# Optimization experiments

Hardware: AMD Instinct MI355X
Metric: run time of the kernel (lower is better)

Reference implementation:

```python
import math
import jax, jax.numpy as jnp
import numpy as np

COULOMB = 14.399645478425668  # eV*Angstrom / e^2


def setup_inputs() -> dict:
    key = jax.random.key(0)
    k0, k1, k2, k3, k4 = jax.random.split(key, 5)
    B, n, F, S = 128, 512, 64, 4  # molecules, atoms/molecule, feat dim, n species
    N = B * n
    node_features = jax.random.normal(k0, (N, F), dtype=jnp.float32)
    pos = jax.random.normal(k1, (N, 3), dtype=jnp.float32) * 5.0  # spread atoms out
    atom_type = jax.random.randint(k2, (N,), 0, S)
    total_charge = jnp.zeros((B, 1), dtype=jnp.float32)
    chi_weight = jax.random.normal(k3, (F, 1), dtype=jnp.float32) / np.float32(np.sqrt(F))
    hardness_param = jnp.ones((S,), dtype=jnp.float32)
    sigma = 0.3 + 0.5 * jax.random.uniform(k4, (S,), dtype=jnp.float32)  # covalent radii
    return dict(node_features=node_features, pos=pos, atom_type=atom_type,
                total_charge=total_charge, chi_weight=chi_weight,
                hardness_param=hardness_param, sigma=sigma, n_per_mol=n)


def reference(node_features, pos, atom_type, total_charge, chi_weight,
              hardness_param, sigma, n_per_mol):
    n = n_per_mol
    N, F = node_features.shape
    B = N // n

    feats = node_features.reshape(B, n, F)
    pos_b = pos.reshape(B, n, 3)
    sp = atom_type.reshape(B, n)

    chi = (feats @ chi_weight)[..., 0]                      # [B, n] electronegativity
    hard = jnp.square(hardness_param)[sp]                   # [B, n]
    sig = sigma[sp]                                         # [B, n]

    # pairwise distances within each molecule (diag masked for safe divide)
    diff = pos_b[:, :, None, :] - pos_b[:, None, :, :]      # [B, n, n, 3]
    d2 = jnp.sum(diff * diff, axis=-1)
    eye = jnp.eye(n, dtype=pos.dtype)
    d = jnp.sqrt(jnp.where(eye, 1.0, d2))                   # [B, n, n]

    gamma = jnp.sqrt(sig[:, :, None] ** 2 + sig[:, None, :] ** 2)
    off = COULOMB * jax.lax.erf(d / (math.sqrt(2.0) * gamma)) / d
    diag = hard + COULOMB / (math.sqrt(math.pi) * sig)      # [B, n]
    coeffs = off * (1.0 - eye) + eye * diag[:, :, None]     # [B, n, n]

    # augmented Qeq system with charge-conservation Lagrange multiplier
    A = jnp.ones((B, n + 1, n + 1), dtype=coeffs.dtype)
    A = A.at[:, :n, :n].set(coeffs)
    A = A.at[:, n, n].set(0.0)
    rhs = jnp.concatenate([-chi, total_charge], axis=1)     # [B, n+1]
    sol = jnp.linalg.solve(A, rhs[..., None])[..., 0]
    q = sol[:, :n]                                          # [B, n] charges

    # E = sum_{i<j} C_ij q_i q_j + sum_i (chi_i q_i + 0.5 diag_i q_i^2)
    #   = 0.5 q^T C q + chi . q   (C includes diagonal)
    e_qeq = 0.5 * jnp.einsum('bi,bij,bj->b', q, coeffs, q) + jnp.sum(chi * q, axis=1)
    return e_qeq[:, None], q.reshape(N, 1)
```

## Files before the change

### kernel.cpp

```cpp
#include <hip/hip_runtime.h>
#include <math.h>

#define NA 512
#define NN (NA*NA)
#define COULOMB 14.399645478425668f
#define SQRT_PI 1.7724538509055160273f

__device__ __forceinline__ float rl(float x, int lane) {
    return __int_as_float(__builtin_amdgcn_readlane(__float_as_int(x), lane));
}

__device__ __forceinline__ float pair_val(float dx, float dy, float dz,
                                          float s2i, float s2k) {
    float d2 = dx*dx + dy*dy + dz*dz;
    float rinv = rsqrtf(d2);
    return COULOMB * erff(d2 * rinv * rsqrtf(2.f * (s2i + s2k))) * rinv;
}

__global__ void k_pre(const float* __restrict__ feats, const float* __restrict__ w,
                      const int* __restrict__ type, const float* __restrict__ hard,
                      const float* __restrict__ sigma,
                      float* __restrict__ chi, float* __restrict__ diag,
                      float* __restrict__ sigA, int N) {
    __shared__ float wl[64];
    int tid = threadIdx.x;
    if (tid < 64) wl[tid] = w[tid];
    __syncthreads();
    int i = blockIdx.x * 256 + tid;
    if (i >= N) return;
    const float4* fp = (const float4*)(feats + (size_t)i * 64);
    float acc = 0.f;
#pragma unroll
    for (int q = 0; q < 16; q++) {
        float4 v = fp[q];
        acc += v.x * wl[4*q] + v.y * wl[4*q+1] + v.z * wl[4*q+2] + v.w * wl[4*q+3];
    }
    chi[i] = acc;
    int t = type[i];
    float s = sigma[t];
    float h = hard[t];
    sigA[i] = s;
    diag[i] = h * h + COULOMB / (SQRT_PI * s);
}

__global__ void __launch_bounds__(256, 1) k_panel(const float* __restrict__ pos,
                                                  const float* __restrict__ sigA,
                                                  const float* __restrict__ diagA,
                                                  float* __restrict__ C, const int j) {
    const int q = blockIdx.x;
    const int b = blockIdx.y;
    float* __restrict__ Cb = C + (size_t)b * NN;
    const int jb = j * 64;
    const int m = NA - jb - 64;
    const int tid = threadIdx.x;
    __shared__ float D[64 * 65];
    __shared__ float DT[64 * 64];
    __shared__ float invd[64];
    __shared__ float px[NA], py[NA], pz[NA], s2s[NA];

    if (j == 0) {
#pragma unroll
        for (int e = 0; e < 2; e++) {
            int i = e * 256 + tid;
            px[i] = pos[((size_t)b * NA + i) * 3 + 0];
            py[i] = pos[((size_t)b * NA + i) * 3 + 1];
            pz[i] = pos[((size_t)b * NA + i) * 3 + 2];
            float s = sigA[b * NA + i];
            s2s[i] = s * s;
        }
        __syncthreads();
    }

#pragma unroll
    for (int e = 0; e < 16; e++) {
        int f = e * 256 + tid;
        int rr = f >> 6, cc = f & 63;
        float v;
        if (j == 0) {
            if (rr == cc) v = diagA[b * NA + rr];
            else v = pair_val(px[rr]-px[cc], py[rr]-py[cc], pz[rr]-pz[cc], s2s[rr], s2s[cc]);
        } else {
            v = Cb[(size_t)(jb + rr) * NA + jb + cc];
        }
        D[rr * 65 + cc] = v;
    }

    const int h = m >> 1;
    const int r0 = q ? h : 0;
    const int nr = q ? (m - h) : h;
    const int r = tid - 32;
    const bool hasrow = (r >= 0 && r < nr);
    const int grow = jb + 64 + r0 + r;
    float rv[64];
    if (hasrow) {
        if (j == 0) {
#pragma unroll
            for (int k = 0; k < 64; k++)
                rv[k] = pair_val(px[grow]-px[k], py[grow]-py[k], pz[grow]-pz[k],
                                 s2s[grow], s2s[k]);
        } else {
            const float4* rp = (const float4*)(Cb + (size_t)grow * NA + jb);
#pragma unroll
            for (int qq = 0; qq < 16; qq++) {
                float4 v = rp[qq];
                rv[4*qq] = v.x; rv[4*qq+1] = v.y; rv[4*qq+2] = v.z; rv[4*qq+3] = v.w;
            }
        }
    }
    __syncthreads();

    if (tid < 64) {
        const int t = tid;
        float cl[64];
#pragma unroll
        for (int i = 0; i < 64; i++) cl[i] = (i >= t) ? D[i * 65 + t] : D[t * 65 + i];
#pragma unroll
        for (int k = 0; k < 64; k++) {
            float pivot = rl(cl[k], k);
            float invp = 1.0f / pivot;
            float factor = (t > k) ? (cl[k] * invp) : 0.0f;
#pragma unroll
            for (int i = k + 1; i < 64; i++) {
                float bc = rl(cl[i], k);
                cl[i] -= bc * factor;
            }
        }
        float rs = 1.0f / sqrtf(cl[t]);
        invd[t] = rs;
#pragma unroll
        for (int i = 0; i < 64; i++)
            if (i >= t) D[i * 65 + t] = cl[i] * rs;
    }
    __syncthreads();

#pragma unroll
    for (int e = 0; e < 16; e++) {
        int f = e * 256 + tid;
        int row = f >> 6, cc = f & 63;
        float v = D[row * 65 + cc];
        DT[row * 64 + cc] = (cc < row) ? v : 0.f;
        if (q == 0 && cc <= row) Cb[(size_t)(jb + row) * NA + jb + cc] = v;
    }
    __syncthreads();

    if (hasrow) {
#pragma unroll
        for (int k = 0; k < 64; k++) {
            float acc = rv[k];
            const float4* Lr = (const float4*)(DT + k * 64);
            const int k4 = k >> 2;
#pragma unroll
            for (int t4 = 0; t4 < k4; t4++) {
                float4 Lv = Lr[t4];
                acc -= Lv.x * rv[4*t4] + Lv.y * rv[4*t4+1] + Lv.z * rv[4*t4+2] + Lv.w * rv[4*t4+3];
            }
#pragma unroll
            for (int tt = k4 * 4; tt < k; tt++) acc -= DT[k * 64 + tt] * rv[tt];
            rv[k] = acc * invd[k];
        }
        float4* rp = (float4*)(Cb + (size_t)grow * NA + jb);
#pragma unroll
        for (int qq = 0; qq < 16; qq++)
            rp[qq] = make_float4(rv[4*qq], rv[4*qq+1], rv[4*qq+2], rv[4*qq+3]);
    }
}

template<bool GEN>
__global__ void __launch_bounds__(256, 3) k_trail(float* __restrict__ C,
                                                  const float* __restrict__ pos,
                                                  const float* __restrict__ sigA,
                                                  const float* __restrict__ diagA,
                                                  const int j) {
    const int b = blockIdx.y;
    float* __restrict__ Cb = C + (size_t)b * NN;
    const int jb = j * 64;
    const int m = NA - jb - 64;
    int t = blockIdx.x;
    int RI = 0;
    while (t >= RI + 1) { t -= RI + 1; RI++; }
    const int RJ = t;
    const int RB = RI * 128, CB = RJ * 128;
    const int vr = min(128, m - RB);
    const int vc = min(128, m - CB);
    const int tid = threadIdx.x;
    const int rg = tid >> 4, cg = tid & 15;

    __shared__ float As[128 * 65];
    __shared__ float Bs[128 * 65];

    float acc[8][8];

    if (GEN) {
        __shared__ float pAx[128], pAy[128], pAz[128], sA[128], dA[128];
        __shared__ float pBx[128], pBy[128], pBz[128], sB[128];
        if (tid < 128) {
            if (RB + tid < m) {
                int ga = b * NA + jb + 64 + RB + tid;
                pAx[tid] = pos[(size_t)ga * 3 + 0];
                pAy[tid] = pos[(size_t)ga * 3 + 1];
                pAz[tid] = pos[(size_t)ga * 3 + 2];
                float s = sigA[ga]; sA[tid] = s * s;
                dA[tid] = diagA[ga];
            }
        } else {
            int u = tid - 128;
            if (CB + u < m) {
                int gb = b * NA + jb + 64 + CB + u;
                pBx[u] = pos[(size_t)gb * 3 + 0];
                pBy[u] = pos[(size_t)gb * 3 + 1];
                pBz[u] = pos[(size_t)gb * 3 + 2];
                float s = sigA[gb]; sB[u] = s * s;
            }
        }
        __syncthreads();
#pragma unroll
        for (int rr = 0; rr < 8; rr++) {
            int row = rg * 8 + rr;
#pragma unroll
            for (int cc = 0; cc < 8; cc++) {
                int col = cg + 16 * cc;
                if (RB + row == CB + col)
                    acc[rr][cc] = dA[row];
                else
                    acc[rr][cc] = pair_val(pAx[row]-pBx[col], pAy[row]-pBy[col],
                                           pAz[row]-pBz[col], sA[row], sB[col]);
            }
        }
        __syncthreads();
    } else {
        const int GRB = jb + 64 + RB, GCB = jb + 64 + CB;
#pragma unroll
        for (int rr = 0; rr < 8; rr++) {
            int row = rg * 8 + rr;
#pragma unroll
            for (int cc = 0; cc < 8; cc++) {
                int col = cg + 16 * cc;
                acc[rr][cc] = (row < vr && col < vc)
                    ? Cb[(size_t)(GRB + row) * NA + GCB + col] : 0.f;
            }
        }
    }

    const float* Pan = Cb + (size_t)(jb + 64) * NA + jb;
#pragma unroll
    for (int e = 0; e < 8; e++) {
        int f = e * 256 + tid;
        int row = f >> 4, s = f & 15;
        float4 v = make_float4(0.f, 0.f, 0.f, 0.f);
        if (row < vr) v = *(const float4*)(Pan + (size_t)(RB + row) * NA + s * 4);
        As[row * 65 + s * 4 + 0] = v.x;
        As[row * 65 + s * 4 + 1] = v.y;
        As[row * 65 + s * 4 + 2] = v.z;
        As[row * 65 + s * 4 + 3] = v.w;
        float4 u = make_float4(0.f, 0.f, 0.f, 0.f);
        if (row < vc) u = *(const float4*)(Pan + (size_t)(CB + row) * NA + s * 4);
        Bs[row * 65 + s * 4 + 0] = u.x;
        Bs[row * 65 + s * 4 + 1] = u.y;
        Bs[row * 65 + s * 4 + 2] = u.z;
        Bs[row * 65 + s * 4 + 3] = u.w;
    }
    __syncthreads();

#pragma unroll 4
    for (int k = 0; k < 64; k++) {
        float ai[8], bj[8];
#pragma unroll
        for (int rr = 0; rr < 8; rr++) ai[rr] = As[(rg * 8 + rr) * 65 + k];
#pragma unroll
        for (int cc = 0; cc < 8; cc++) bj[cc] = Bs[(cg + 16 * cc) * 65 + k];
#pragma unroll
        for (int rr = 0; rr < 8; rr++)
#pragma unroll
            for (int cc = 0; cc < 8; cc++)
                acc[rr][cc] = fmaf(-ai[rr], bj[cc], acc[rr][cc]);
    }

    const int GRB = jb + 64 + RB, GCB = jb + 64 + CB;
#pragma unroll
    for (int rr = 0; rr < 8; rr++) {
        int row = rg * 8 + rr;
        if (row < vr) {
#pragma unroll
            for (int cc = 0; cc < 8; cc++) {
                int col = cg + 16 * cc;
                if (col < vc)
                    Cb[(size_t)(GRB + row) * NA + GCB + col] = acc[rr][cc];
            }
        }
    }
}

__global__ void __launch_bounds__(512, 1) k_solve2(const float* __restrict__ C,
                                                   const float* __restrict__ chiA,
                                                   float* __restrict__ x1out,
                                                   float* __restrict__ x2out) {
    const int b = blockIdx.x;
    const int rhs = blockIdx.y;
    const float* Cb = C + (size_t)b * NN;
    const int tid = threadIdx.x;
    __shared__ float D[64 * 65];
    __shared__ float r[NA];
    __shared__ float pb[4][NA];

    r[tid] = rhs ? 1.0f : chiA[b * NA + tid];

    const int sub = tid & 7;
    const int rowg = tid >> 3;

    for (int j = 0; j < 8; j++) {
        const int jb = j * 64;
        __syncthreads();
#pragma unroll
        for (int e = 0; e < 8; e++) {
            int f = e * 512 + tid;
            int row = f >> 6, cc = f & 63;
            D[row * 65 + cc] = Cb[(size_t)(jb + row) * NA + jb + cc];
        }
        __syncthreads();
        if (tid < 64) {
            float val = r[jb + tid];
            float idg = 1.0f / D[tid * 65 + tid];
#pragma unroll
            for (int k = 0; k < 64; k++) {
                float yk = rl(val, k) * rl(idg, k);
                if (tid == k) r[jb + k] = yk;
                float lv = (tid > k) ? D[tid * 65 + k] : 0.f;
                val -= lv * yk;
            }
        }
        __syncthreads();
#pragma unroll
        for (int p = 0; p < 7; p++) {
            int g = jb + 64 + p * 64 + rowg;
            if (g < NA) {
                const float4* Lr = (const float4*)(Cb + (size_t)g * NA + jb + sub * 8);
                float4 a0 = Lr[0], a1 = Lr[1];
                int y0 = jb + sub * 8;
                float d1 = a0.x*r[y0]   + a0.y*r[y0+1] + a0.z*r[y0+2] + a0.w*r[y0+3]
                         + a1.x*r[y0+4] + a1.y*r[y0+5] + a1.z*r[y0+6] + a1.w*r[y0+7];
                d1 += __shfl_xor(d1, 1);
                d1 += __shfl_xor(d1, 2);
                d1 += __shfl_xor(d1, 4);
                if (sub == 0) r[g] -= d1;
            }
        }
    }

    const int ii = tid & 127;
    const int gg = tid >> 7;
    for (int j = 7; j >= 0; j--) {
        const int jb = j * 64;
        __syncthreads();
#pragma unroll
        for (int e = 0; e < 8; e++) {
            int f = e * 512 + tid;
            int row = f >> 6, cc = f & 63;
            D[row * 65 + cc] = Cb[(size_t)(jb + row) * NA + jb + cc];
        }
        __syncthreads();
        if (tid < 64) {
            float val = r[jb + tid];
            float idg = 1.0f / D[tid * 65 + tid];
#pragma unroll
            for (int k = 63; k >= 0; k--) {
                float xk = rl(val, k) * rl(idg, k);
                if (tid == k) r[jb + k] = xk;
                float lv = (tid < k) ? D[k * 65 + tid] : 0.f;
                val -= lv * xk;
            }
        }
        __syncthreads();
        if (jb > 0) {
            const int nf4 = jb >> 2;
            float4 s1 = make_float4(0.f, 0.f, 0.f, 0.f);
            if (ii < nf4) {
#pragma unroll
                for (int gq = 0; gq < 16; gq++) {
                    int g = jb + gg * 16 + gq;
                    float x1 = r[g];
                    float4 Lv = *(const float4*)(Cb + (size_t)g * NA + ii * 4);
                    s1.x += Lv.x * x1; s1.y += Lv.y * x1; s1.z += Lv.z * x1; s1.w += Lv.w * x1;
                }
            }
            *(float4*)(&pb[gg][ii * 4]) = s1;
            __syncthreads();
            if (tid < jb)
                r[tid] -= pb[0][tid] + pb[1][tid] + pb[2][tid] + pb[3][tid];
        }
    }
    __syncthreads();

    float* xo = rhs ? x2out : x1out;
    xo[(size_t)b * NA + tid] = r[tid];
}

__global__ void __launch_bounds__(512, 1) k_final(const float* __restrict__ x1,
                                                  const float* __restrict__ x2,
                                                  const float* __restrict__ chiA,
                                                  const float* __restrict__ Qtot,
                                                  float* __restrict__ out, int B) {
    const int b = blockIdx.x;
    const int tid = threadIdx.x;
    __shared__ float red[16];
    __shared__ float muS;

    float v1 = x1[(size_t)b * NA + tid];
    float v2 = x2[(size_t)b * NA + tid];

    float s1p = v1, s2p = v2;
#pragma unroll
    for (int off = 1; off < 64; off <<= 1) {
        s1p += __shfl_xor(s1p, off);
        s2p += __shfl_xor(s2p, off);
    }
    if ((tid & 63) == 0) { red[tid >> 6] = s1p; red[8 + (tid >> 6)] = s2p; }
    __syncthreads();
    if (tid == 0) {
        float s1 = 0.f, s2 = 0.f;
#pragma unroll
        for (int wv = 0; wv < 8; wv++) { s1 += red[wv]; s2 += red[8 + wv]; }
        muS = -(Qtot[b] + s1) / s2;
    }
    __syncthreads();
    float mu = muS;
    float qv = -v1 - mu * v2;
    out[B + (size_t)b * NA + tid] = qv;

    float eacc = chiA[b * NA + tid] * qv;
#pragma unroll
    for (int off = 1; off < 64; off <<= 1) eacc += __shfl_xor(eacc, off);
    __syncthreads();
    if ((tid & 63) == 0) red[tid >> 6] = eacc;
    __syncthreads();
    if (tid == 0) {
        float e = 0.f;
#pragma unroll
        for (int wv = 0; wv < 8; wv++) e += red[wv];
        out[b] = 0.5f * e - 0.5f * mu * Qtot[b];
    }
}

extern "C" void kernel_launch(void* const* d_in, const int* in_sizes, int n_in,
                              void* d_out, int out_size, void* d_ws, size_t ws_size,
                              hipStream_t stream) {
    const int B = in_sizes[3];
    const int N = in_sizes[2];
    const float* feats = (const float*)d_in[0];
    const float* pos   = (const float*)d_in[1];
    const int*   type  = (const int*)d_in[2];
    const float* Qt    = (const float*)d_in[3];
    const float* w     = (const float*)d_in[4];
    const float* hard  = (const float*)d_in[5];
    const float* sig   = (const float*)d_in[6];
    float* out = (float*)d_out;
    float* ws  = (float*)d_ws;

    float* C    = ws;
    float* chi  = ws + (size_t)B * NN;
    float* diag = chi + N;
    float* sigA = diag + N;

    k_pre<<<(N + 255) / 256, 256, 0, stream>>>(feats, w, type, hard, sig, chi, diag, sigA, N);

    static const int tilesJ[7] = {10, 6, 6, 3, 3, 1, 1};
    for (int j = 0; j < 8; j++) {
        k_panel<<<dim3(2, B), 256, 0, stream>>>(pos, sigA, diag, C, j);
        if (j < 7) {
            if (j == 0)
                k_trail<true><<<dim3(tilesJ[j], B), 256, 0, stream>>>(C, pos, sigA, diag, j);
            else
                k_trail<false><<<dim3(tilesJ[j], B), 256, 0, stream>>>(C, pos, sigA, diag, j);
        }
    }
    k_solve2<<<dim3(B, 2), 512, 0, stream>>>(C, chi, diag, sigA);
    k_final<<<B, 512, 0, stream>>>(diag, sigA, chi, Qt, out, B);
}
```

Baseline: 749.8 us.

## Fuse forward substitution into Cholesky panel kernel, leaving only back-substitution

```diff
diff --git a/kernel.cpp b/kernel.cpp
--- a/kernel.cpp
+++ b/kernel.cpp
@@ -21,7 +21,8 @@
                       const int* __restrict__ type, const float* __restrict__ hard,
                       const float* __restrict__ sigma,
                       float* __restrict__ chi, float* __restrict__ diag,
-                      float* __restrict__ sigA, int N) {
+                      float* __restrict__ sigA,
+                      float* __restrict__ r1, float* __restrict__ r2, int N) {
     __shared__ float wl[64];
     int tid = threadIdx.x;
     if (tid < 64) wl[tid] = w[tid];
@@ -36,6 +37,8 @@
         acc += v.x * wl[4*q] + v.y * wl[4*q+1] + v.z * wl[4*q+2] + v.w * wl[4*q+3];
     }
     chi[i] = acc;
+    r1[i] = acc;
+    r2[i] = 1.0f;
     int t = type[i];
     float s = sigma[t];
     float h = hard[t];
@@ -46,7 +49,9 @@
 __global__ void __launch_bounds__(256, 1) k_panel(const float* __restrict__ pos,
                                                   const float* __restrict__ sigA,
                                                   const float* __restrict__ diagA,
-                                                  float* __restrict__ C, const int j) {
+                                                  float* __restrict__ C,
+                                                  float* __restrict__ r1,
+                                                  float* __restrict__ r2, const int j) {
     const int q = blockIdx.x;
     const int b = blockIdx.y;
     float* __restrict__ Cb = C + (size_t)b * NN;
@@ -56,6 +61,7 @@
     __shared__ float D[64 * 65];
     __shared__ float DT[64 * 64];
     __shared__ float invd[64];
+    __shared__ float y1s[64], y2s[64];
     __shared__ float px[NA], py[NA], pz[NA], s2s[NA];
 
     if (j == 0) {
@@ -130,6 +136,25 @@
 #pragma unroll
         for (int i = 0; i < 64; i++)
             if (i >= t) D[i * 65 + t] = cl[i] * rs;
+
+        float v1 = r1[(size_t)b * NA + jb + t];
+        float v2 = r2[(size_t)b * NA + jb + t];
+#pragma unroll
+        for (int k = 0; k < 64; k++) {
+            float rsk = rl(rs, k);
+            float y1k = rl(v1, k) * rsk;
+            float y2k = rl(v2, k) * rsk;
+            if (t == k) {
+                y1s[t] = y1k; y2s[t] = y2k;
+                if (q == 0) {
+                    r1[(size_t)b * NA + jb + t] = y1k;
+                    r2[(size_t)b * NA + jb + t] = y2k;
+                }
+            }
+            float lv = (t > k) ? D[t * 65 + k] : 0.f;
+            v1 -= lv * y1k;
+            v2 -= lv * y2k;
+        }
     }
     __syncthreads();
 
@@ -162,6 +187,15 @@
 #pragma unroll
         for (int qq = 0; qq < 16; qq++)
             rp[qq] = make_float4(rv[4*qq], rv[4*qq+1], rv[4*qq+2], rv[4*qq+3]);
+
+        float a1 = 0.f, a2 = 0.f;
+#pragma unroll
+        for (int k = 0; k < 64; k++) {
+            a1 = fmaf(rv[k], y1s[k], a1);
+            a2 = fmaf(rv[k], y2s[k], a2);
+        }
+        r1[(size_t)b * NA + grow] -= a1;
+        r2[(size_t)b * NA + grow] -= a2;
     }
 }
 
@@ -290,10 +324,9 @@
     }
 }
 
-__global__ void __launch_bounds__(512, 1) k_solve2(const float* __restrict__ C,
-                                                   const float* __restrict__ chiA,
-                                                   float* __restrict__ x1out,
-                                                   float* __restrict__ x2out) {
+__global__ void __launch_bounds__(512, 1) k_back(const float* __restrict__ C,
+                                                 float* __restrict__ r1g,
+                                                 float* __restrict__ r2g) {
     const int b = blockIdx.x;
     const int rhs = blockIdx.y;
     const float* Cb = C + (size_t)b * NN;
@@ -302,49 +335,8 @@
     __shared__ float r[NA];
     __shared__ float pb[4][NA];
 
-    r[tid] = rhs ? 1.0f : chiA[b * NA + tid];
-
-    const int sub = tid & 7;
-    const int rowg = tid >> 3;
-
-    for (int j = 0; j < 8; j++) {
-        const int jb = j * 64;
-        __syncthreads();
-#pragma unroll
-        for (int e = 0; e < 8; e++) {
-            int f = e * 512 + tid;
-            int row = f >> 6, cc = f & 63;
-            D[row * 65 + cc] = Cb[(size_t)(jb + row) * NA + jb + cc];
-        }
-        __syncthreads();
-        if (tid < 64) {
-            float val = r[jb + tid];
-            float idg = 1.0f / D[tid * 65 + tid];
-#pragma unroll
-            for (int k = 0; k < 64; k++) {
-                float yk = rl(val, k) * rl(idg, k);
-                if (tid == k) r[jb + k] = yk;
-                float lv = (tid > k) ? D[tid * 65 + k] : 0.f;
-                val -= lv * yk;
-            }
-        }
-        __syncthreads();
-#pragma unroll
-        for (int p = 0; p < 7; p++) {
-            int g = jb + 64 + p * 64 + rowg;
-            if (g < NA) {
-                const float4* Lr = (const float4*)(Cb + (size_t)g * NA + jb + sub * 8);
-                float4 a0 = Lr[0], a1 = Lr[1];
-                int y0 = jb + sub * 8;
-                float d1 = a0.x*r[y0]   + a0.y*r[y0+1] + a0.z*r[y0+2] + a0.w*r[y0+3]
-                         + a1.x*r[y0+4] + a1.y*r[y0+5] + a1.z*r[y0+6] + a1.w*r[y0+7];
-                d1 += __shfl_xor(d1, 1);
-                d1 += __shfl_xor(d1, 2);
-                d1 += __shfl_xor(d1, 4);
-                if (sub == 0) r[g] -= d1;
-            }
-        }
-    }
+    float* rg = rhs ? r2g : r1g;
+    r[tid] = rg[(size_t)b * NA + tid];
 
     const int ii = tid & 127;
     const int gg = tid >> 7;
@@ -390,8 +382,7 @@
     }
     __syncthreads();
 
-    float* xo = rhs ? x2out : x1out;
-    xo[(size_t)b * NA + tid] = r[tid];
+    rg[(size_t)b * NA + tid] = r[tid];
 }
 
 __global__ void __launch_bounds__(512, 1) k_final(const float* __restrict__ x1,
@@ -459,12 +450,15 @@
     float* chi  = ws + (size_t)B * NN;
     float* diag = chi + N;
     float* sigA = diag + N;
-
-    k_pre<<<(N + 255) / 256, 256, 0, stream>>>(feats, w, type, hard, sig, chi, diag, sigA, N);
+    float* r1   = sigA + N;
+    float* r2   = r1 + N;
+
+    k_pre<<<(N + 255) / 256, 256, 0, stream>>>(feats, w, type, hard, sig,
+                                               chi, diag, sigA, r1, r2, N);
 
     static const int tilesJ[7] = {10, 6, 6, 3, 3, 1, 1};
     for (int j = 0; j < 8; j++) {
-        k_panel<<<dim3(2, B), 256, 0, stream>>>(pos, sigA, diag, C, j);
+        k_panel<<<dim3(2, B), 256, 0, stream>>>(pos, sigA, diag, C, r1, r2, j);
         if (j < 7) {
             if (j == 0)
                 k_trail<true><<<dim3(tilesJ[j], B), 256, 0, stream>>>(C, pos, sigA, diag, j);
@@ -472,6 +466,6 @@
                 k_trail<false><<<dim3(tilesJ[j], B), 256, 0, stream>>>(C, pos, sigA, diag, j);
         }
     }
-    k_solve2<<<dim3(B, 2), 512, 0, stream>>>(C, chi, diag, sigA);
-    k_final<<<B, 512, 0, stream>>>(diag, sigA, chi, Qt, out, B);
-}
+    k_back<<<dim3(B, 2), 512, 0, stream>>>(C, r1, r2);
+    k_final<<<B, 512, 0, stream>>>(r1, r2, chi, Qt, out, B);
+}
```

New measurement: 745.4 us. No clear change (-0.6%).
